# Optimization experiments

Measured on AMD Instinct MI355X. Metric: run time of the kernel, lower is better.

## Reference

```python
import jax, jax.numpy as jnp
import numpy as np

NC, NK, K, PAD, SCALE, MID = 3, 64, 3, 1, 4, 4
K2, S2 = K * K, SCALE * SCALE
B, H, W = 4, 128, 128


def conv2d(x, w, b, pad):
    y = jax.lax.conv_general_dilated(x, w, (1, 1), [(pad, pad), (pad, pad)],
                                     dimension_numbers=('NCHW', 'OIHW', 'NCHW'))
    return y + b[None, :, None, None]


def bilinear_gather(x, py, px):
    # x: [B,C,H,W]; py/px: [B,K2,H,W] absolute (fractional) sample coords; zero outside.
    b, c, h, w = x.shape
    y0, x0 = jnp.floor(py), jnp.floor(px)
    wy, wx = py - y0, px - x0
    xf = x.reshape(b, c, h * w)

    def g(yi, xi):
        valid = ((yi >= 0) & (yi <= h - 1) & (xi >= 0) & (xi <= w - 1)).astype(x.dtype)
        yc = jnp.clip(yi, 0, h - 1).astype(jnp.int32)
        xc = jnp.clip(xi, 0, w - 1).astype(jnp.int32)
        idx = (yc * w + xc).reshape(b, -1)
        v = jax.vmap(lambda a, i: a[:, i])(xf, idx).reshape(b, c, *yi.shape[1:])
        return v * valid[:, None]

    return (((1 - wy) * (1 - wx))[:, None] * g(y0, x0)
            + ((1 - wy) * wx)[:, None] * g(y0, x0 + 1)
            + (wy * (1 - wx))[:, None] * g(y0 + 1, x0)
            + (wy * wx)[:, None] * g(y0 + 1, x0 + 1))


def deform_conv(x, ow, ob, mw, mb, w, b):
    # DCNv2: offsets [B,2*K2,H,W] (y,x interleaved per tap), modulation mask 2*sigmoid.
    bsz, c, h, ww = x.shape
    off = conv2d(x, ow, ob, PAD).reshape(bsz, K2, 2, h, ww)
    mask = 2.0 * jax.nn.sigmoid(conv2d(x, mw, mb, PAD))  # [B,K2,H,W]
    ky, kx = jnp.meshgrid(jnp.arange(K), jnp.arange(K), indexing='ij')
    py = jnp.arange(h)[None, None, :, None] + (ky.reshape(K2) - PAD)[None, :, None, None] + off[:, :, 0]
    px = jnp.arange(ww)[None, None, None, :] + (kx.reshape(K2) - PAD)[None, :, None, None] + off[:, :, 1]
    patches = bilinear_gather(x, py, px) * mask[:, None]  # [B,C,K2,H,W]
    return jnp.einsum('bckhw,ock->bohw', patches, w.reshape(w.shape[0], c, K2)) + b[None, :, None, None]


def convlstm(x, h, c, w, b):
    g = conv2d(jnp.concatenate([x, h], 1), w, b, PAD)
    i, f, o, gg = jnp.split(g, 4, axis=1)
    c = jax.nn.sigmoid(f) * c + jax.nn.sigmoid(i) * jnp.tanh(gg)
    return jax.nn.sigmoid(o) * jnp.tanh(c), c


def ddf_up(x, sp_w, sp_b, ch_w1, ch_b1, ch_w2, ch_b2):
    # DDFUpPack: S2 branches, per-pixel spatial filter + SE-style per-channel filter,
    # 'add' combine, per-branch dynamic KxK filtering, then pixel_shuffle(SCALE).
    bsz, c, h, w = x.shape
    sp = conv2d(x, sp_w.reshape(S2 * K2, c, K, K), sp_b.reshape(S2 * K2), PAD).reshape(bsz, S2, K2, h, w)
    pooled = x.mean((2, 3))  # global avg pool -> [B,C]
    h1 = jax.nn.relu(jnp.einsum('bc,smc->bsm', pooled, ch_w1) + ch_b1[None])
    ch = (jnp.einsum('bsm,skm->bsk', h1, ch_w2) + ch_b2[None]).reshape(bsz, S2, c, K2)
    xp = jnp.pad(x, ((0, 0), (0, 0), (PAD, PAD), (PAD, PAD)))
    patches = jnp.stack([xp[:, :, i:i + h, j:j + w] for i in range(K) for j in range(K)], 2)  # [B,C,K2,H,W]
    filt = ch[:, :, :, :, None, None] + sp[:, :, None]  # [B,S2,C,K2,H,W]
    out = jnp.einsum('bckhw,bsckhw->bcshw', patches, filt)  # [B,C,S2,H,W]
    out = out.reshape(bsz, c, SCALE, SCALE, h, w).transpose(0, 1, 4, 2, 5, 3)
    return out.reshape(bsz, c, h * SCALE, w * SCALE)  # pixel_shuffle


def _forward(X, lstm_w, lstm_b,
             d1_ow, d1_ob, d1_mw, d1_mb, d1_w, d1_b,
             d2_ow, d2_ob, d2_mw, d2_mb, d2_w, d2_b,
             d3_ow, d3_ob, d3_mw, d3_mb, d3_w, d3_b,
             conv_w, conv_b, sp_w, sp_b, ch_w1, ch_b1, ch_w2, ch_b2):
    lr = X
    bsz, _, h, w = X.shape
    z = jnp.zeros((bsz, NK, h, w), X.dtype)
    hid, cell = convlstm(X, z, z, lstm_w, lstm_b)
    x = deform_conv(jnp.concatenate([hid, lr], 1), d1_ow, d1_ob, d1_mw, d1_mb, d1_w, d1_b)
    x = deform_conv(jnp.concatenate([x, lr], 1), d2_ow, d2_ob, d2_mw, d2_mb, d2_w, d2_b)
    x = deform_conv(jnp.concatenate([x, lr], 1), d3_ow, d3_ob, d3_mw, d3_mb, d3_w, d3_b)
    x = conv2d(jnp.concatenate([x, lr], 1), conv_w, conv_b, PAD)
    out = jnp.clip(ddf_up(x, sp_w, sp_b, ch_w1, ch_b1, ch_w2, ch_b2), 0.0, 255.0)
    return out, hid, cell


def setup_inputs():
    key = jax.random.key(0)
    ks = iter(jax.random.split(key, 40))

    def p(shape, s=0.05):
        return jax.random.normal(next(ks), shape, jnp.float32) * s

    cin = NK + NC
    d = {'X': jax.random.normal(next(ks), (B, NC, H, W), jnp.float32),
         'lstm_w': p((4 * NK, NC + NK, K, K)), 'lstm_b': p((4 * NK,))}
    for i in (1, 2, 3):
        d[f'd{i}_ow'] = p((2 * K2, cin, K, K)); d[f'd{i}_ob'] = p((2 * K2,))
        d[f'd{i}_mw'] = p((K2, cin, K, K));     d[f'd{i}_mb'] = p((K2,))
        d[f'd{i}_w'] = p((NK, cin, K, K));      d[f'd{i}_b'] = p((NK,))
    d['conv_w'] = p((NC, cin, K, K)); d['conv_b'] = p((NC,))
    d['sp_w'] = p((S2, K2, NC, K, K)); d['sp_b'] = p((S2, K2))
    d['ch_w1'] = p((S2, MID, NC)); d['ch_b1'] = p((S2, MID))
    d['ch_w2'] = p((S2, NC * K2, MID)); d['ch_b2'] = p((S2, NC * K2))
    return d


def reference(X, lstm_w, lstm_b,
              d1_ow, d1_ob, d1_mw, d1_mb, d1_w, d1_b,
              d2_ow, d2_ob, d2_mw, d2_mb, d2_w, d2_b,
              d3_ow, d3_ob, d3_mw, d3_mb, d3_w, d3_b,
              conv_w, conv_b, sp_w, sp_b, ch_w1, ch_b1, ch_w2, ch_b2):
    return _forward(X, lstm_w, lstm_b,
                    d1_ow, d1_ob, d1_mw, d1_mb, d1_w, d1_b,
                    d2_ow, d2_ob, d2_mw, d2_mb, d2_w, d2_b,
                    d3_ow, d3_ob, d3_mw, d3_mb, d3_w, d3_b,
                    conv_w, conv_b, sp_w, sp_b, ch_w1, ch_b1, ch_w2, ch_b2)
```

## Files before the change

kernel.cpp:

```cpp
#include <hip/hip_runtime.h>
#include <hip/hip_bf16.h>
#include <math.h>

#define NC 3
#define NK 64
#define KK 3
#define K2 9
#define PAD 1
#define SCALE 4
#define S2 16
#define MID 4
#define B 4
#define H 128
#define W 128
#define HW (H*W)
#define CIN 67
#define OUT_HW (H*SCALE)
#define CST 64

typedef short bf16x8 __attribute__((ext_vector_type(8)));
typedef float f32x4 __attribute__((ext_vector_type(4)));
typedef float f32x2 __attribute__((ext_vector_type(2)));
typedef unsigned int u32x4 __attribute__((ext_vector_type(4)));
typedef unsigned int u32x2 __attribute__((ext_vector_type(2)));

__device__ __forceinline__ float fast_sigmoid(float v) { return 1.f / (1.f + __expf(-v)); }
__device__ __forceinline__ float fast_tanh(float v) { return 2.f / (1.f + __expf(-2.f * v)) - 1.f; }

__device__ __forceinline__ unsigned short f2bf(float f) {
    unsigned int u = __float_as_uint(f);
    unsigned int r = (u + 0x7FFFu + ((u >> 16) & 1u)) >> 16;
    return (unsigned short)r;
}

__device__ __forceinline__ f32x2 unpk(unsigned int u) {
    f32x2 r;
    r[0] = __uint_as_float(u << 16);
    r[1] = __uint_as_float(u & 0xffff0000u);
    return r;
}

__device__ __forceinline__ void load_patch(const float* __restrict__ xc, int y, int x, float* p) {
#pragma unroll
    for (int dy = -1; dy <= 1; dy++) {
#pragma unroll
        for (int dx = -1; dx <= 1; dx++) {
            int yy = y + dy, xx = x + dx;
            float v = (yy >= 0 && yy < H && xx >= 0 && xx < W) ? xc[yy * W + xx] : 0.f;
            p[(dy + 1) * 3 + (dx + 1)] = v;
        }
    }
}

__global__ void k_prepL(const float* __restrict__ lw, unsigned short* __restrict__ aplk) {
    int g = blockIdx.x;
    int tid = threadIdx.x;
    int lane = tid >> 3, j = tid & 7;
    int o = g * 16 + (lane & 15);
    int k = ((lane >> 4) << 3) + j;
    float val = 0.f;
    if (k < 27) {
        int c = k / 9, tap = k % 9;
        int gate = o >> 6, nk = o & 63;
        int base = (gate == 0) ? 0 : (gate == 1) ? 2 * NK : 3 * NK;
        val = lw[(size_t)(base + nk) * (CIN * 9) + c * 9 + tap];
    }
    aplk[(size_t)g * 512 + tid] = f2bf(val);
}

__global__ __launch_bounds__(256, 4) void k_lstm(const float* __restrict__ X,
                                                 const unsigned short* __restrict__ aplk,
                                                 const float* __restrict__ lb,
                                                 unsigned short* __restrict__ xcatA,
                                                 float* __restrict__ hid_out,
                                                 float* __restrict__ cell_out,
                                                 float* __restrict__ lrp) {
    int tid = threadIdx.x;
    int lane = tid & 63;
    int nt = __builtin_amdgcn_readfirstlane(tid >> 6);
    int blk = blockIdx.x;
    int sg = (blk & 7) * 128 + (blk >> 3);
    int b = sg >> 8;
    int hwbase = (sg & 255) * 64;
    int n = lane & 15, q = lane >> 4;
    int hw = hwbase + nt * 16 + n;
    int y = hw >> 7, x = hw & (W - 1);

    if (nt == 0) {
        int px = hwbase + lane;
        f32x4 v = {X[(size_t)(b * NC + 0) * HW + px], X[(size_t)(b * NC + 1) * HW + px],
                   X[(size_t)(b * NC + 2) * HW + px], 0.f};
        *(f32x4*)(lrp + ((size_t)b * HW + px) * 4) = v;
    }

    bf16x8 bf;
#pragma unroll
    for (int j = 0; j < 8; j++) {
        int k = q * 8 + j;
        float v = 0.f;
        if (k < 27) {
            int c = k / 9, tap = k % 9;
            int ky = tap / 3, kx = tap % 3;
            int yy = y + ky - 1, xx = x + kx - 1;
            if (yy >= 0 && yy < H && xx >= 0 && xx < W)
                v = X[(size_t)(b * NC + c) * HW + yy * W + xx];
        }
        bf[j] = (short)f2bf(v);
    }

    f32x4 acc[12];
#pragma unroll
    for (int mt = 0; mt < 12; mt++) { f32x4 z = {0.f, 0.f, 0.f, 0.f}; acc[mt] = z; }
#pragma unroll
    for (int mt = 0; mt < 12; mt++) {
        bf16x8 af = *(const bf16x8*)(aplk + (size_t)mt * 512 + lane * 8);
        acc[mt] = __builtin_amdgcn_mfma_f32_16x16x32_bf16(af, bf, acc[mt], 0, 0, 0);
    }

    unsigned short* xo = xcatA + (size_t)b * HW * CST;
#pragma unroll
    for (int mt = 0; mt < 4; mt++) {
        float hv4[4];
#pragma unroll
        for (int r = 0; r < 4; r++) {
            int nk = mt * 16 + q * 4 + r;
            float gi = acc[mt][r] + lb[nk];
            float go = acc[mt + 4][r] + lb[2 * NK + nk];
            float gg = acc[mt + 8][r] + lb[3 * NK + nk];
            float cv = fast_sigmoid(gi) * fast_tanh(gg);
            float hv = fast_sigmoid(go) * fast_tanh(cv);
            hv4[r] = hv;
            hid_out[(size_t)(b * NK + nk) * HW + hw] = hv;
            cell_out[(size_t)(b * NK + nk) * HW + hw] = cv;
        }
        u32x2 st;
        st[0] = (unsigned int)f2bf(hv4[0]) | ((unsigned int)f2bf(hv4[1]) << 16);
        st[1] = (unsigned int)f2bf(hv4[2]) | ((unsigned int)f2bf(hv4[3]) << 16);
        int p = 2 * mt + (q >> 1);
        *(u32x2*)(xo + (((size_t)p * HW + hw) << 3) + (q & 1) * 4) = st;
    }
}

__global__ void k_prepA(const float* __restrict__ w, unsigned short* __restrict__ apk) {
    int g = blockIdx.x;
    int tid = threadIdx.x;
    int lane = tid >> 3, j = tid & 7;
    int mt = g & 3, r = g >> 2;
    int ks = r % 3, tap = r / 3;
    int o = mt * 16 + (lane & 15);
    int c = ks * 32 + ((lane >> 4) << 3) + j;
    float val = (c < CIN) ? w[(size_t)o * (CIN * 9) + c * 9 + tap] : 0.f;
    apk[(size_t)g * 512 + tid] = f2bf(val);
}

__global__ void k_prepOM(const float* __restrict__ ow, const float* __restrict__ mw,
                         unsigned short* __restrict__ apk) {
    int g = blockIdx.x;
    int tid = threadIdx.x;
    int lane = tid >> 3, j = tid & 7;
    int mt = g & 1, r = g >> 1;
    int kss = r % 3, tap = r / 3;
    int o = mt * 16 + (lane & 15);
    int c = kss * 32 + ((lane >> 4) << 3) + j;
    float val = 0.f;
    if (c < CIN) {
        if (o < 18) val = ow[(size_t)o * (CIN * 9) + c * 9 + tap];
        else if (o < 27) val = mw[(size_t)(o - 18) * (CIN * 9) + c * 9 + tap];
    }
    apk[(size_t)g * 512 + tid] = f2bf(val);
}

__global__ __launch_bounds__(256, 4) void k_offdef(const unsigned short* __restrict__ xcat,
                                                   const float* __restrict__ lrp,
                                                   const unsigned short* __restrict__ apkom,
                                                   const float* __restrict__ ob,
                                                   const float* __restrict__ mb,
                                                   const unsigned short* __restrict__ apk,
                                                   const float* __restrict__ bias,
                                                   unsigned short* __restrict__ xout) {
    __shared__ float somp[4][16][37];
    int tid = threadIdx.x;
    int lane = tid & 63;
    int wid = __builtin_amdgcn_readfirstlane(tid >> 6);
    int blk = blockIdx.x;
    int sg = (blk & 7) * 128 + (blk >> 3);
    int b = sg >> 8;
    int hwbase = (sg & 255) * 64;
    int n = lane & 15, q = lane >> 4;
    int hw = hwbase + wid * 16 + n;
    int y = hw >> 7, x = hw & (W - 1);

    const unsigned short* xb = xcat + (size_t)b * HW * CST;
    const unsigned short* pl0 = xb + (((size_t)q * HW) << 3);
    const unsigned short* pl1 = xb + (((size_t)(4 + q) * HW) << 3);
    const float* lb_ = lrp + (size_t)b * HW * 4;

    {
        f32x4 acc2[2];
#pragma unroll
        for (int mt = 0; mt < 2; mt++) { f32x4 z = {0.f, 0.f, 0.f, 0.f}; acc2[mt] = z; }
#pragma unroll
        for (int tap = 0; tap < K2; tap++) {
            int ky = tap / 3, kx = tap - ky * 3;
            int yy = y + ky - 1, xx = x + kx - 1;
            bool vld = (yy >= 0 && yy < H && xx >= 0 && xx < W);
            int ii = min(max(yy, 0), H - 1) * W + min(max(xx, 0), W - 1);
            const unsigned short* ab = apkom + (size_t)(tap * 6) * 512 + lane * 8;
            {
                bf16x8 bfv = *(const bf16x8*)(pl0 + ((size_t)ii << 3));
                if (!vld) { bf16x8 z = {0, 0, 0, 0, 0, 0, 0, 0}; bfv = z; }
#pragma unroll
                for (int mt = 0; mt < 2; mt++) {
                    bf16x8 af = *(const bf16x8*)(ab + (size_t)(0 * 2 + mt) * 512);
                    acc2[mt] = __builtin_amdgcn_mfma_f32_16x16x32_bf16(af, bfv, acc2[mt], 0, 0, 0);
                }
            }
            {
                bf16x8 bfv = *(const bf16x8*)(pl1 + ((size_t)ii << 3));
                if (!vld) { bf16x8 z = {0, 0, 0, 0, 0, 0, 0, 0}; bfv = z; }
#pragma unroll
                for (int mt = 0; mt < 2; mt++) {
                    bf16x8 af = *(const bf16x8*)(ab + (size_t)(1 * 2 + mt) * 512);
                    acc2[mt] = __builtin_amdgcn_mfma_f32_16x16x32_bf16(af, bfv, acc2[mt], 0, 0, 0);
                }
            }
            bf16x8 bf2 = {0, 0, 0, 0, 0, 0, 0, 0};
            if (q == 0 && vld) {
                f32x4 L = *(const f32x4*)(lb_ + ((size_t)ii << 2));
#pragma unroll
                for (int j = 0; j < 4; j++) bf2[j] = (short)f2bf(L[j]);
            }
#pragma unroll
            for (int mt = 0; mt < 2; mt++) {
                bf16x8 af = *(const bf16x8*)(ab + (size_t)(4 + mt) * 512);
                acc2[mt] = __builtin_amdgcn_mfma_f32_16x16x32_bf16(af, bf2, acc2[mt], 0, 0, 0);
            }
        }
#pragma unroll
        for (int mt = 0; mt < 2; mt++)
#pragma unroll
            for (int r = 0; r < 4; r++) {
                int o = mt * 16 + q * 4 + r;
                float s = acc2[mt][r];
                if (o < 18)
                    somp[wid][n][(o >> 1) * 4 + (o & 1)] = s + ob[o];
                else if (o < 27)
                    somp[wid][n][(o - 18) * 4 + 2] = 2.f * fast_sigmoid(s + mb[o - 18]);
            }
    }
    __syncthreads();

    f32x4 acc[4];
#pragma unroll
    for (int mt = 0; mt < 4; mt++) { f32x4 z = {0.f, 0.f, 0.f, 0.f}; acc[mt] = z; }

#pragma unroll
    for (int tap = 0; tap < K2; tap++) {
        float omy = somp[wid][n][tap * 4 + 0];
        float omx = somp[wid][n][tap * 4 + 1];
        float m = somp[wid][n][tap * 4 + 2];
        int ky = tap / 3, kx = tap - ky * 3;
        float py = (float)(y + ky - 1) + omy;
        float px_ = (float)(x + kx - 1) + omx;
        float fy = floorf(py), fx = floorf(px_);
        float wy = py - fy, wx = px_ - fx;
        int y0 = (int)fy, x0 = (int)fx;
        int y1 = y0 + 1, x1 = x0 + 1;
        float vy0 = (y0 >= 0 && y0 <= H - 1) ? 1.f : 0.f;
        float vy1 = (y1 >= 0 && y1 <= H - 1) ? 1.f : 0.f;
        float vx0 = (x0 >= 0 && x0 <= W - 1) ? 1.f : 0.f;
        float vx1 = (x1 >= 0 && x1 <= W - 1) ? 1.f : 0.f;
        int yc0 = min(max(y0, 0), H - 1), yc1 = min(max(y1, 0), H - 1);
        int xc0 = min(max(x0, 0), W - 1), xc1 = min(max(x1, 0), W - 1);
        float a00 = (1.f - wy) * (1.f - wx) * m * vy0 * vx0;
        float a01 = (1.f - wy) * wx * m * vy0 * vx1;
        float a10 = wy * (1.f - wx) * m * vy1 * vx0;
        float a11 = wy * wx * m * vy1 * vx1;
        int j00 = yc0 * W + xc0, j01 = yc0 * W + xc1;
        int j10 = yc1 * W + xc0, j11 = yc1 * W + xc1;

        const unsigned short* ab = apk + (size_t)(tap * 12) * 512 + lane * 8;
        {
            u32x4 d00 = *(const u32x4*)(pl0 + ((size_t)j00 << 3));
            u32x4 d01 = *(const u32x4*)(pl0 + ((size_t)j01 << 3));
            u32x4 d10 = *(const u32x4*)(pl0 + ((size_t)j10 << 3));
            u32x4 d11 = *(const u32x4*)(pl0 + ((size_t)j11 << 3));
            bf16x8 bf;
            unsigned int* bfu = (unsigned int*)&bf;
#pragma unroll
            for (int e = 0; e < 4; e++) {
                f32x2 v = unpk(d00[e]) * a00 + unpk(d01[e]) * a01
                        + unpk(d10[e]) * a10 + unpk(d11[e]) * a11;
                bfu[e] = (unsigned int)f2bf(v[0]) | ((unsigned int)f2bf(v[1]) << 16);
            }
#pragma unroll
            for (int mt = 0; mt < 4; mt++) {
                bf16x8 af = *(const bf16x8*)(ab + (size_t)(0 * 4 + mt) * 512);
                acc[mt] = __builtin_amdgcn_mfma_f32_16x16x32_bf16(af, bf, acc[mt], 0, 0, 0);
            }
        }
        {
            u32x4 d00 = *(const u32x4*)(pl1 + ((size_t)j00 << 3));
            u32x4 d01 = *(const u32x4*)(pl1 + ((size_t)j01 << 3));
            u32x4 d10 = *(const u32x4*)(pl1 + ((size_t)j10 << 3));
            u32x4 d11 = *(const u32x4*)(pl1 + ((size_t)j11 << 3));
            bf16x8 bf;
            unsigned int* bfu = (unsigned int*)&bf;
#pragma unroll
            for (int e = 0; e < 4; e++) {
                f32x2 v = unpk(d00[e]) * a00 + unpk(d01[e]) * a01
                        + unpk(d10[e]) * a10 + unpk(d11[e]) * a11;
                bfu[e] = (unsigned int)f2bf(v[0]) | ((unsigned int)f2bf(v[1]) << 16);
            }
#pragma unroll
            for (int mt = 0; mt < 4; mt++) {
                bf16x8 af = *(const bf16x8*)(ab + (size_t)(1 * 4 + mt) * 512);
                acc[mt] = __builtin_amdgcn_mfma_f32_16x16x32_bf16(af, bf, acc[mt], 0, 0, 0);
            }
        }
        bf16x8 bf2 = {0, 0, 0, 0, 0, 0, 0, 0};
        if (q == 0) {
            f32x4 L00 = *(const f32x4*)(lb_ + ((size_t)j00 << 2));
            f32x4 L01 = *(const f32x4*)(lb_ + ((size_t)j01 << 2));
            f32x4 L10 = *(const f32x4*)(lb_ + ((size_t)j10 << 2));
            f32x4 L11 = *(const f32x4*)(lb_ + ((size_t)j11 << 2));
            f32x4 Lv = L00 * a00 + L01 * a01 + L10 * a10 + L11 * a11;
#pragma unroll
            for (int j = 0; j < 4; j++) bf2[j] = (short)f2bf(Lv[j]);
        }
#pragma unroll
        for (int mt = 0; mt < 4; mt++) {
            bf16x8 af = *(const bf16x8*)(ab + (size_t)(2 * 4 + mt) * 512);
            acc[mt] = __builtin_amdgcn_mfma_f32_16x16x32_bf16(af, bf2, acc[mt], 0, 0, 0);
        }
    }

    unsigned short* xo = xout + (size_t)b * HW * CST;
#pragma unroll
    for (int mt = 0; mt < 4; mt++) {
        float s[4];
#pragma unroll
        for (int r = 0; r < 4; r++) {
            int o = mt * 16 + q * 4 + r;
            s[r] = acc[mt][r] + bias[o];
        }
        u32x2 st;
        st[0] = (unsigned int)f2bf(s[0]) | ((unsigned int)f2bf(s[1]) << 16);
        st[1] = (unsigned int)f2bf(s[2]) | ((unsigned int)f2bf(s[3]) << 16);
        int p = 2 * mt + (q >> 1);
        *(u32x2*)(xo + (((size_t)p * HW + hw) << 3) + (q & 1) * 4) = st;
    }
}

__global__ __launch_bounds__(256, 4) void k_conv3(const unsigned short* __restrict__ xcat,
                                                  const float* __restrict__ lrp,
                                                  const float* __restrict__ cw,
                                                  const float* __restrict__ cb,
                                                  float* __restrict__ y3) {
    __shared__ float red[4 * 3 * 64];
    int tid = threadIdx.x;
    int lane = tid & 63;
    int wid = __builtin_amdgcn_readfirstlane(tid >> 6);
    int blk = blockIdx.x;
    int sg = (blk & 7) * 128 + (blk >> 3);
    int b = sg >> 8;
    int hwbase = (sg & 255) * 64;
    int hw = hwbase + lane;
    int y = hw >> 7, x = hw & (W - 1);
    int t0 = (wid == 0) ? 0 : 3 + (wid - 1) * 2;
    int t1 = (wid == 0) ? 3 : t0 + 2;

    float a0 = 0.f, a1 = 0.f, a2 = 0.f;
    const unsigned short* xb = xcat + (size_t)b * HW * CST;
    const float* lb_ = lrp + (size_t)b * HW * 4;
#pragma unroll 1
    for (int tap = t0; tap < t1; tap++) {
        int ky = tap / 3, kx = tap - ky * 3;
        int yy = y + ky - 1, xx = x + kx - 1;
        if (yy < 0 || yy >= H || xx < 0 || xx >= W) continue;
        int ii = yy * W + xx;
#pragma unroll
        for (int c8 = 0; c8 < 8; c8++) {
            u32x4 d = *(const u32x4*)(xb + (((size_t)c8 * HW + ii) << 3));
#pragma unroll
            for (int e = 0; e < 4; e++) {
                int c = c8 * 8 + e * 2;
                float lo = __uint_as_float(d[e] << 16);
                float hi = __uint_as_float(d[e] & 0xffff0000u);
                a0 += lo * cw[0 * (CIN * 9) + c * 9 + tap] + hi * cw[0 * (CIN * 9) + (c + 1) * 9 + tap];
                a1 += lo * cw[1 * (CIN * 9) + c * 9 + tap] + hi * cw[1 * (CIN * 9) + (c + 1) * 9 + tap];
                a2 += lo * cw[2 * (CIN * 9) + c * 9 + tap] + hi * cw[2 * (CIN * 9) + (c + 1) * 9 + tap];
            }
        }
        f32x4 L = *(const f32x4*)(lb_ + ((size_t)ii << 2));
#pragma unroll
        for (int e = 0; e < 3; e++) {
            a0 += L[e] * cw[0 * (CIN * 9) + (64 + e) * 9 + tap];
            a1 += L[e] * cw[1 * (CIN * 9) + (64 + e) * 9 + tap];
            a2 += L[e] * cw[2 * (CIN * 9) + (64 + e) * 9 + tap];
        }
    }
    red[(wid * 3 + 0) * 64 + lane] = a0;
    red[(wid * 3 + 1) * 64 + lane] = a1;
    red[(wid * 3 + 2) * 64 + lane] = a2;
    __syncthreads();
    if (tid < 192) {
        int oc = tid >> 6, px = tid & 63;
        float s = red[(0 * 3 + oc) * 64 + px] + red[(1 * 3 + oc) * 64 + px]
                + red[(2 * 3 + oc) * 64 + px] + red[(3 * 3 + oc) * 64 + px];
        y3[(size_t)(b * NC + oc) * HW + hwbase + px] = s + cb[oc];
    }
}

__global__ __launch_bounds__(256) void k_pool(const float* __restrict__ y3,
                                              float* __restrict__ pooled) {
    int bc = blockIdx.x;
    const float* p = y3 + (size_t)bc * HW;
    float s = 0.f;
    for (int i = threadIdx.x; i < HW; i += 256) s += p[i];
    __shared__ float red[256];
    red[threadIdx.x] = s;
    __syncthreads();
    for (int off = 128; off > 0; off >>= 1) {
        if (threadIdx.x < off) red[threadIdx.x] += red[threadIdx.x + off];
        __syncthreads();
    }
    if (threadIdx.x == 0) pooled[bc] = red[0] / (float)HW;
}

__global__ __launch_bounds__(256) void k_ddf(const float* __restrict__ y3,
                                             const float* __restrict__ spw,
                                             const float* __restrict__ spb,
                                             const float* __restrict__ pooled,
                                             const float* __restrict__ ch_w1,
                                             const float* __restrict__ ch_b1,
                                             const float* __restrict__ ch_w2,
                                             const float* __restrict__ ch_b2,
                                             float* __restrict__ out) {
    __shared__ float s_spw[4 * K2 * NC * 9];
    __shared__ float s_spb[4 * K2];
    __shared__ float s_ch[4 * NC * K2];
    int t = blockIdx.x * blockDim.x + threadIdx.x;
    int b = t >> 14, hw = t & (HW - 1), y = hw >> 7, x = hw & (W - 1);
    int s0 = blockIdx.y * 4;
    for (int i = threadIdx.x; i < 4 * K2 * NC * 9; i += 256) s_spw[i] = spw[s0 * K2 * NC * 9 + i];
    if (threadIdx.x < 4 * K2) s_spb[threadIdx.x] = spb[s0 * K2 + threadIdx.x];
    if (threadIdx.x < 4 * NC * K2) {
        int t2 = threadIdx.x;
        int si = t2 / (NC * K2), kk = t2 - si * (NC * K2);
        int s = s0 + si;
        float a = ch_b2[s * (NC * K2) + kk];
#pragma unroll
        for (int m = 0; m < MID; m++) {
            float h1 = ch_b1[s * MID + m];
#pragma unroll
            for (int c = 0; c < NC; c++) h1 += pooled[b * NC + c] * ch_w1[(s * MID + m) * NC + c];
            a += fmaxf(h1, 0.f) * ch_w2[(s * (NC * K2) + kk) * MID + m];
        }
        s_ch[t2] = a;
    }
    __syncthreads();
    float p[NC][9];
#pragma unroll
    for (int c = 0; c < NC; c++) load_patch(y3 + (b * NC + c) * HW, y, x, p[c]);
#pragma unroll
    for (int si = 0; si < 4; si++) {
        int s = s0 + si;
        float spv[K2];
#pragma unroll
        for (int k = 0; k < K2; k++) {
            float a = s_spb[si * K2 + k];
            const float* w = s_spw + (si * K2 + k) * (NC * 9);
#pragma unroll
            for (int c = 0; c < NC; c++)
#pragma unroll
                for (int tt = 0; tt < 9; tt++) a += p[c][tt] * w[c * 9 + tt];
            spv[k] = a;
        }
        int sy = s >> 2, sx = s & 3;
#pragma unroll
        for (int c = 0; c < NC; c++) {
            float a = 0.f;
            const float* chp = s_ch + (si * NC + c) * K2;
#pragma unroll
            for (int k = 0; k < K2; k++) a += p[c][k] * (chp[k] + spv[k]);
            a = fminf(fmaxf(a, 0.f), 255.f);
            out[((size_t)(b * NC + c) * OUT_HW + (y * SCALE + sy)) * OUT_HW + (x * SCALE + sx)] = a;
        }
    }
}

extern "C" void kernel_launch(void* const* d_in, const int* in_sizes, int n_in,
                              void* d_out, int out_size, void* d_ws, size_t ws_size,
                              hipStream_t stream) {
    const float* X = (const float*)d_in[0];
    const float* lstm_w = (const float*)d_in[1];
    const float* lstm_b = (const float*)d_in[2];
    const float* ow[3] = {(const float*)d_in[3], (const float*)d_in[9], (const float*)d_in[15]};
    const float* ob[3] = {(const float*)d_in[4], (const float*)d_in[10], (const float*)d_in[16]};
    const float* mw[3] = {(const float*)d_in[5], (const float*)d_in[11], (const float*)d_in[17]};
    const float* mb[3] = {(const float*)d_in[6], (const float*)d_in[12], (const float*)d_in[18]};
    const float* dw[3] = {(const float*)d_in[7], (const float*)d_in[13], (const float*)d_in[19]};
    const float* db[3] = {(const float*)d_in[8], (const float*)d_in[14], (const float*)d_in[20]};
    const float* conv_w = (const float*)d_in[21];
    const float* conv_b = (const float*)d_in[22];
    const float* sp_w = (const float*)d_in[23];
    const float* sp_b = (const float*)d_in[24];
    const float* ch_w1 = (const float*)d_in[25];
    const float* ch_b1 = (const float*)d_in[26];
    const float* ch_w2 = (const float*)d_in[27];
    const float* ch_b2 = (const float*)d_in[28];

    float* out = (float*)d_out;
    const size_t OUT_IMG = (size_t)B * NC * OUT_HW * OUT_HW;
    const size_t HIDSZ = (size_t)B * NK * HW;
    float* hid_out = out + OUT_IMG;
    float* cell_out = out + OUT_IMG + HIDSZ;

    float* ws = (float*)d_ws;
    const size_t XCATF = (size_t)B * HW * CST / 2;
    unsigned short* xcatA = (unsigned short*)ws;  ws += XCATF;
    unsigned short* xcatB = (unsigned short*)ws;  ws += XCATF;
    float* lrp = ws;              ws += (size_t)B * HW * 4;
    unsigned short* apk[3];
    for (int i = 0; i < 3; i++) { apk[i] = (unsigned short*)ws; ws += 108 * 512 / 2; }
    unsigned short* apkOM[3];
    for (int i = 0; i < 3; i++) { apkOM[i] = (unsigned short*)ws; ws += 54 * 512 / 2; }
    unsigned short* aplk = (unsigned short*)ws;  ws += 12 * 512 / 2;
    float* y3 = ws;               ws += (size_t)B * NC * HW;
    float* pooled = ws;           ws += 16;

    dim3 blk(256);
    dim3 g4(B * HW / 256, 4);
    dim3 gd(B * HW / 64);

    k_prepL<<<dim3(12), dim3(512), 0, stream>>>(lstm_w, aplk);
    for (int i = 0; i < 3; i++) {
        k_prepA<<<dim3(108), dim3(512), 0, stream>>>(dw[i], apk[i]);
        k_prepOM<<<dim3(54), dim3(512), 0, stream>>>(ow[i], mw[i], apkOM[i]);
    }
    k_lstm<<<gd, blk, 0, stream>>>(X, aplk, lstm_b, xcatA, hid_out, cell_out, lrp);

    k_offdef<<<gd, blk, 0, stream>>>(xcatA, lrp, apkOM[0], ob[0], mb[0], apk[0], db[0], xcatB);
    k_offdef<<<gd, blk, 0, stream>>>(xcatB, lrp, apkOM[1], ob[1], mb[1], apk[1], db[1], xcatA);
    k_offdef<<<gd, blk, 0, stream>>>(xcatA, lrp, apkOM[2], ob[2], mb[2], apk[2], db[2], xcatB);

    k_conv3<<<gd, blk, 0, stream>>>(xcatB, lrp, conv_w, conv_b, y3);
    k_pool<<<dim3(B * NC), blk, 0, stream>>>(y3, pooled);
    k_ddf<<<g4, blk, 0, stream>>>(y3, sp_w, sp_b, pooled, ch_w1, ch_b1, ch_w2, ch_b2, out);
}
```

Measured before the change: 331.0 us.

## Merge weight-prep launches, fuse pooling into conv3, vectorize DDF output stores

The seven weight-packing launches become one combined k_prep kernel, which also zeroes the pooled accumulator. The separate k_pool reduction is removed: k_conv3 now does a wave shuffle reduction and atomically adds per-channel means into pooled. k_ddf collects its four subpixel outputs per channel and writes them as one 16-byte vector store instead of four scalar stores. These changes cut launch count, a serial low-occupancy reduction pass and uncoalesced writes, at the cost of atomics and nondeterministic float summation order.

```diff
diff --git a/kernel.cpp b/kernel.cpp
--- a/kernel.cpp
+++ b/kernel.cpp
@@ -52,20 +52,63 @@
     }
 }
 
-__global__ void k_prepL(const float* __restrict__ lw, unsigned short* __restrict__ aplk) {
+__global__ void k_prep(const float* __restrict__ lw,
+                       const float* __restrict__ dw0, const float* __restrict__ dw1,
+                       const float* __restrict__ dw2,
+                       const float* __restrict__ ow0, const float* __restrict__ ow1,
+                       const float* __restrict__ ow2,
+                       const float* __restrict__ mw0, const float* __restrict__ mw1,
+                       const float* __restrict__ mw2,
+                       unsigned short* __restrict__ aplk,
+                       unsigned short* __restrict__ apk0, unsigned short* __restrict__ apk1,
+                       unsigned short* __restrict__ apk2,
+                       unsigned short* __restrict__ apkOM0, unsigned short* __restrict__ apkOM1,
+                       unsigned short* __restrict__ apkOM2,
+                       float* __restrict__ pooled) {
     int g = blockIdx.x;
     int tid = threadIdx.x;
     int lane = tid >> 3, j = tid & 7;
-    int o = g * 16 + (lane & 15);
-    int k = ((lane >> 4) << 3) + j;
-    float val = 0.f;
-    if (k < 27) {
-        int c = k / 9, tap = k % 9;
-        int gate = o >> 6, nk = o & 63;
-        int base = (gate == 0) ? 0 : (gate == 1) ? 2 * NK : 3 * NK;
-        val = lw[(size_t)(base + nk) * (CIN * 9) + c * 9 + tap];
-    }
-    aplk[(size_t)g * 512 + tid] = f2bf(val);
+    if (g == 0 && tid < 16) pooled[tid] = 0.f;
+
+    if (g < 12) {
+        int o = g * 16 + (lane & 15);
+        int k = ((lane >> 4) << 3) + j;
+        float val = 0.f;
+        if (k < 27) {
+            int c = k / 9, tap = k % 9;
+            int gate = o >> 6, nk = o & 63;
+            int base = (gate == 0) ? 0 : (gate == 1) ? 2 * NK : 3 * NK;
+            val = lw[(size_t)(base + nk) * (CIN * 9) + c * 9 + tap];
+        }
+        aplk[(size_t)g * 512 + tid] = f2bf(val);
+    } else if (g < 336) {
+        int gi = g - 12;
+        int i = gi / 108, gg = gi - i * 108;
+        const float* w = (i == 0) ? dw0 : (i == 1) ? dw1 : dw2;
+        unsigned short* apk = (i == 0) ? apk0 : (i == 1) ? apk1 : apk2;
+        int mt = gg & 3, r = gg >> 2;
+        int ks = r % 3, tap = r / 3;
+        int o = mt * 16 + (lane & 15);
+        int c = ks * 32 + ((lane >> 4) << 3) + j;
+        float val = (c < CIN) ? w[(size_t)o * (CIN * 9) + c * 9 + tap] : 0.f;
+        apk[(size_t)gg * 512 + tid] = f2bf(val);
+    } else {
+        int gi = g - 336;
+        int i = gi / 54, gg = gi - i * 54;
+        const float* ow = (i == 0) ? ow0 : (i == 1) ? ow1 : ow2;
+        const float* mw = (i == 0) ? mw0 : (i == 1) ? mw1 : mw2;
+        unsigned short* apk = (i == 0) ? apkOM0 : (i == 1) ? apkOM1 : apkOM2;
+        int mt = gg & 1, r = gg >> 1;
+        int kss = r % 3, tap = r / 3;
+        int o = mt * 16 + (lane & 15);
+        int c = kss * 32 + ((lane >> 4) << 3) + j;
+        float val = 0.f;
+        if (c < CIN) {
+            if (o < 18) val = ow[(size_t)o * (CIN * 9) + c * 9 + tap];
+            else if (o < 27) val = mw[(size_t)(o - 18) * (CIN * 9) + c * 9 + tap];
+        }
+        apk[(size_t)gg * 512 + tid] = f2bf(val);
+    }
 }
 
 __global__ __launch_bounds__(256, 4) void k_lstm(const float* __restrict__ X,
@@ -139,35 +182,6 @@
         int p = 2 * mt + (q >> 1);
         *(u32x2*)(xo + (((size_t)p * HW + hw) << 3) + (q & 1) * 4) = st;
     }
-}
-
-__global__ void k_prepA(const float* __restrict__ w, unsigned short* __restrict__ apk) {
-    int g = blockIdx.x;
-    int tid = threadIdx.x;
-    int lane = tid >> 3, j = tid & 7;
-    int mt = g & 3, r = g >> 2;
-    int ks = r % 3, tap = r / 3;
-    int o = mt * 16 + (lane & 15);
-    int c = ks * 32 + ((lane >> 4) << 3) + j;
-    float val = (c < CIN) ? w[(size_t)o * (CIN * 9) + c * 9 + tap] : 0.f;
-    apk[(size_t)g * 512 + tid] = f2bf(val);
-}
-
-__global__ void k_prepOM(const float* __restrict__ ow, const float* __restrict__ mw,
-                         unsigned short* __restrict__ apk) {
-    int g = blockIdx.x;
-    int tid = threadIdx.x;
-    int lane = tid >> 3, j = tid & 7;
-    int mt = g & 1, r = g >> 1;
-    int kss = r % 3, tap = r / 3;
-    int o = mt * 16 + (lane & 15);
-    int c = kss * 32 + ((lane >> 4) << 3) + j;
-    float val = 0.f;
-    if (c < CIN) {
-        if (o < 18) val = ow[(size_t)o * (CIN * 9) + c * 9 + tap];
-        else if (o < 27) val = mw[(size_t)(o - 18) * (CIN * 9) + c * 9 + tap];
-    }
-    apk[(size_t)g * 512 + tid] = f2bf(val);
 }
 
 __global__ __launch_bounds__(256, 4) void k_offdef(const unsigned short* __restrict__ xcat,
@@ -356,7 +370,8 @@
                                                   const float* __restrict__ lrp,
                                                   const float* __restrict__ cw,
                                                   const float* __restrict__ cb,
-                                                  float* __restrict__ y3) {
+                                                  float* __restrict__ y3,
+                                                  float* __restrict__ pooled) {
     __shared__ float red[4 * 3 * 64];
     int tid = threadIdx.x;
     int lane = tid & 63;
@@ -408,24 +423,13 @@
         int oc = tid >> 6, px = tid & 63;
         float s = red[(0 * 3 + oc) * 64 + px] + red[(1 * 3 + oc) * 64 + px]
                 + red[(2 * 3 + oc) * 64 + px] + red[(3 * 3 + oc) * 64 + px];
-        y3[(size_t)(b * NC + oc) * HW + hwbase + px] = s + cb[oc];
-    }
-}
-
-__global__ __launch_bounds__(256) void k_pool(const float* __restrict__ y3,
-                                              float* __restrict__ pooled) {
-    int bc = blockIdx.x;
-    const float* p = y3 + (size_t)bc * HW;
-    float s = 0.f;
-    for (int i = threadIdx.x; i < HW; i += 256) s += p[i];
-    __shared__ float red[256];
-    red[threadIdx.x] = s;
-    __syncthreads();
-    for (int off = 128; off > 0; off >>= 1) {
-        if (threadIdx.x < off) red[threadIdx.x] += red[threadIdx.x + off];
-        __syncthreads();
-    }
-    if (threadIdx.x == 0) pooled[bc] = red[0] / (float)HW;
+        float v = s + cb[oc];
+        y3[(size_t)(b * NC + oc) * HW + hwbase + px] = v;
+        float r = v;
+#pragma unroll
+        for (int off = 32; off > 0; off >>= 1) r += __shfl_xor(r, off);
+        if ((tid & 63) == 0) atomicAdd(&pooled[b * NC + oc], r * (1.f / (float)HW));
+    }
 }
 
 __global__ __launch_bounds__(256) void k_ddf(const float* __restrict__ y3,
@@ -463,9 +467,9 @@
     float p[NC][9];
 #pragma unroll
     for (int c = 0; c < NC; c++) load_patch(y3 + (b * NC + c) * HW, y, x, p[c]);
+    f32x4 ov[NC];
 #pragma unroll
     for (int si = 0; si < 4; si++) {
-        int s = s0 + si;
         float spv[K2];
 #pragma unroll
         for (int k = 0; k < K2; k++) {
@@ -477,17 +481,19 @@
                 for (int tt = 0; tt < 9; tt++) a += p[c][tt] * w[c * 9 + tt];
             spv[k] = a;
         }
-        int sy = s >> 2, sx = s & 3;
 #pragma unroll
         for (int c = 0; c < NC; c++) {
             float a = 0.f;
             const float* chp = s_ch + (si * NC + c) * K2;
 #pragma unroll
             for (int k = 0; k < K2; k++) a += p[c][k] * (chp[k] + spv[k]);
-            a = fminf(fmaxf(a, 0.f), 255.f);
-            out[((size_t)(b * NC + c) * OUT_HW + (y * SCALE + sy)) * OUT_HW + (x * SCALE + sx)] = a;
-        }
-    }
+            ov[c][si] = fminf(fmaxf(a, 0.f), 255.f);
+        }
+    }
+    int sy = s0 >> 2;
+#pragma unroll
+    for (int c = 0; c < NC; c++)
+        *(f32x4*)(out + ((size_t)(b * NC + c) * OUT_HW + (y * SCALE + sy)) * OUT_HW + x * SCALE) = ov[c];
 }
 
 extern "C" void kernel_launch(void* const* d_in, const int* in_sizes, int n_in,
@@ -534,18 +540,16 @@
     dim3 g4(B * HW / 256, 4);
     dim3 gd(B * HW / 64);
 
-    k_prepL<<<dim3(12), dim3(512), 0, stream>>>(lstm_w, aplk);
-    for (int i = 0; i < 3; i++) {
-        k_prepA<<<dim3(108), dim3(512), 0, stream>>>(dw[i], apk[i]);
-        k_prepOM<<<dim3(54), dim3(512), 0, stream>>>(ow[i], mw[i], apkOM[i]);
-    }
+    k_prep<<<dim3(498), dim3(512), 0, stream>>>(
+        lstm_w, dw[0], dw[1], dw[2], ow[0], ow[1], ow[2], mw[0], mw[1], mw[2],
+        aplk, apk[0], apk[1], apk[2], apkOM[0], apkOM[1], apkOM[2], pooled);
+
     k_lstm<<<gd, blk, 0, stream>>>(X, aplk, lstm_b, xcatA, hid_out, cell_out, lrp);
 
     k_offdef<<<gd, blk, 0, stream>>>(xcatA, lrp, apkOM[0], ob[0], mb[0], apk[0], db[0], xcatB);
     k_offdef<<<gd, blk, 0, stream>>>(xcatB, lrp, apkOM[1], ob[1], mb[1], apk[1], db[1], xcatA);
     k_offdef<<<gd, blk, 0, stream>>>(xcatA, lrp, apkOM[2], ob[2], mb[2], apk[2], db[2], xcatB);
 
-    k_conv3<<<gd, blk, 0, stream>>>(xcatB, lrp, conv_w, conv_b, y3);
-    k_pool<<<dim3(B * NC), blk, 0, stream>>>(y3, pooled);
+    k_conv3<<<gd, blk, 0, stream>>>(xcatB, lrp, conv_w, conv_b, y3, pooled);
     k_ddf<<<g4, blk, 0, stream>>>(y3, sp_w, sp_b, pooled, ch_w1, ch_b1, ch_w2, ch_b2, out);
 }
```

After: 345.2 us. 4.3% more time.
